# Performance work log

Hardware: AMD Instinct MI355X
Metric: run time of the kernel (lower is better)

## Reference

```python
import jax, jax.numpy as jnp
import numpy as np

N_NODES = 100000
N_EDGES = 6400000
PENALTY_N = 0.1  # init arg `n`


def setup_inputs() -> dict:
    key = jax.random.key(0)
    k1, k2, k3, k4, k5 = jax.random.split(key, 5)
    edge_index = jax.random.randint(k1, (2, N_EDGES), 0, N_NODES, dtype=jnp.int64 if jax.config.read('jax_enable_x64') else jnp.int32)
    edge_weight = jax.random.uniform(k2, (N_EDGES,), dtype=jnp.float32)
    nodes_yield_rate = jax.random.uniform(k3, (N_NODES,), dtype=jnp.float32)
    nodes_traffic = jax.random.uniform(k4, (N_NODES,), dtype=jnp.float32)
    nodes_cost = jax.random.uniform(k5, (N_NODES,), dtype=jnp.float32)
    return {
        'edge_index': edge_index,
        'edge_weight': edge_weight,
        'nodes_yield_rate': nodes_yield_rate,
        'nodes_traffic': nodes_traffic,
        'nodes_cost': nodes_cost,
    }


def reference(edge_index, edge_weight, nodes_yield_rate, nodes_traffic, nodes_cost):
    # Original loop reads src/dst traffic from the ORIGINAL tensor and accumulates
    # updates into a clone; both branches are equivalent to:
    #   src -= |diff| * n * w ; dst += |diff| * n * w
    # i.e. a pure per-edge scatter-add with no edge-order dependency.
    src = edge_index[0]
    dst = edge_index[1]
    diff = nodes_traffic[src] - nodes_traffic[dst]          # [E]
    transfer = jnp.abs(diff) * PENALTY_N * edge_weight      # [E]
    new_traffic = nodes_traffic.at[src].add(-transfer).at[dst].add(transfer)
    total_service_efficiency = jnp.sum(nodes_yield_rate * new_traffic - nodes_cost)
    return new_traffic, total_service_efficiency
```

## Files before the change

### kernel.cpp

```cpp
#include <hip/hip_runtime.h>

#define PENALTY_N 0.1f
#define CP 33344
#define HPAD 64
#define MAX_BPP 85
#define ABLK 1024

__global__ __launch_bounds__(ABLK, 4) void part_scatter_kernel(
    const int* __restrict__ src_idx,
    const int* __restrict__ dst_idx,
    const float* __restrict__ w,
    const float* __restrict__ traffic,
    float* __restrict__ scratch,
    float* __restrict__ out_scalar,
    int nE, int nN, int Bpp) {
    __shared__ float hist[CP + HPAD];

    const int p = blockIdx.x / Bpp;
    const int b = blockIdx.x % Bpp;
    const int lo = p * CP;
    const unsigned csz = (unsigned)min(CP, nN - lo);
    const int tid = threadIdx.x;

    if (blockIdx.x == 0 && tid == 0) *out_scalar = 0.0f;

    {
        float4* h4 = (float4*)hist;
        const int n4 = (CP + HPAD) / 4;
        for (int i = tid; i < n4; i += ABLK)
            h4[i] = make_float4(0.f, 0.f, 0.f, 0.f);
    }
    __syncthreads();

    const int nvec = nE >> 2;
    const int4* __restrict__ src4 = (const int4*)src_idx;
    const int4* __restrict__ dst4 = (const int4*)dst_idx;
    const float4* __restrict__ w4 = (const float4*)w;
    const int stride = Bpp * ABLK;

    for (int v = b * ABLK + tid; v < nvec; v += stride) {
        int4 s = src4[v];
        int4 d = dst4[v];
        float4 ww = w4[v];

        #pragma unroll
        for (int k = 0; k < 4; ++k) {
            int si = (&s.x)[k];
            int di = (&d.x)[k];
            unsigned so = (unsigned)(si - lo);
            unsigned doo = (unsigned)(di - lo);
            bool inS = so < csz;
            bool inD = doo < csz;
            if (inS || inD) {
                float t = fabsf(traffic[si] - traffic[di]) * (PENALTY_N * (&ww.x)[k]);
                unsigned iS = inS ? so : (unsigned)CP;
                unsigned iD = inD ? doo : (unsigned)CP;
                atomicAdd(&hist[iS], -t);
                atomicAdd(&hist[iD], t);
            }
        }
    }
    for (int e = (nvec << 2) + b * ABLK + tid; e < nE; e += stride) {
        int si = src_idx[e];
        int di = dst_idx[e];
        unsigned so = (unsigned)(si - lo);
        unsigned doo = (unsigned)(di - lo);
        bool inS = so < csz;
        bool inD = doo < csz;
        if (inS || inD) {
            float t = fabsf(traffic[si] - traffic[di]) * (PENALTY_N * w[e]);
            unsigned iS = inS ? so : (unsigned)CP;
            unsigned iD = inD ? doo : (unsigned)CP;
            atomicAdd(&hist[iS], -t);
            atomicAdd(&hist[iD], t);
        }
    }

    __syncthreads();
    float* dst = scratch + (size_t)blockIdx.x * CP;
    {
        const int n4 = (int)(csz >> 2);
        float4* d4 = (float4*)dst;
        const float4* h4 = (const float4*)hist;
        for (int i = tid; i < n4; i += ABLK) d4[i] = h4[i];
        for (int i = (n4 << 2) + tid; i < (int)csz; i += ABLK) dst[i] = hist[i];
    }
}

__global__ __launch_bounds__(256) void part_reduce_kernel(
    const float* __restrict__ scratch,
    const float* __restrict__ traffic,
    const float* __restrict__ yield_rate,
    const float* __restrict__ cost,
    float* __restrict__ out,
    int nN, int Bpp) {
    const int tid = blockIdx.x * blockDim.x + threadIdx.x;
    const int stride = gridDim.x * blockDim.x;

    float acc = 0.0f;
    for (int i = tid; i < nN; i += stride) {
        int p = i / CP;
        int off = i - p * CP;
        const float* base = scratch + (size_t)p * Bpp * CP + off;

        float s0 = traffic[i], s1 = 0.0f, s2 = 0.0f, s3 = 0.0f;
        int b = 0;
        for (; b + 8 <= Bpp; b += 8) {
            const float* q = base + (size_t)b * CP;
            float a0 = q[0 * (size_t)CP];
            float a1 = q[1 * (size_t)CP];
            float a2 = q[2 * (size_t)CP];
            float a3 = q[3 * (size_t)CP];
            float a4 = q[4 * (size_t)CP];
            float a5 = q[5 * (size_t)CP];
            float a6 = q[6 * (size_t)CP];
            float a7 = q[7 * (size_t)CP];
            s0 += a0 + a4;
            s1 += a1 + a5;
            s2 += a2 + a6;
            s3 += a3 + a7;
        }
        for (; b < Bpp; ++b) s0 += base[(size_t)b * CP];
        float s = (s0 + s1) + (s2 + s3);
        out[i] = s;
        acc = fmaf(yield_rate[i], s, acc) - cost[i];
    }

    #pragma unroll
    for (int off = 32; off > 0; off >>= 1) acc += __shfl_down(acc, off, 64);

    __shared__ float wsum[4];
    const int lane = threadIdx.x & 63;
    const int wid = threadIdx.x >> 6;
    if (lane == 0) wsum[wid] = acc;
    __syncthreads();
    if (threadIdx.x == 0)
        atomicAdd(&out[nN], wsum[0] + wsum[1] + wsum[2] + wsum[3]);
}

__global__ void init_out_kernel(const float* __restrict__ traffic,
                                float* __restrict__ out, int nN) {
    int i = blockIdx.x * blockDim.x + threadIdx.x;
    if (i < nN) out[i] = traffic[i];
    else if (i == nN) out[i] = 0.0f;
}

__global__ __launch_bounds__(256) void edge_scatter_kernel(
    const int* __restrict__ src_idx, const int* __restrict__ dst_idx,
    const float* __restrict__ w, const float* __restrict__ traffic,
    float* __restrict__ out, int nE) {
    const int tid = blockIdx.x * blockDim.x + threadIdx.x;
    const int stride = gridDim.x * blockDim.x;
    for (int e = tid; e < nE; e += stride) {
        int s = src_idx[e];
        int d = dst_idx[e];
        float t = fabsf(traffic[s] - traffic[d]) * (PENALTY_N * w[e]);
        atomicAdd(&out[s], -t);
        atomicAdd(&out[d], t);
    }
}

__global__ __launch_bounds__(256) void reduce_kernel(
    const float* __restrict__ new_traffic, const float* __restrict__ yield_rate,
    const float* __restrict__ cost, float* __restrict__ total, int nN) {
    const int tid = blockIdx.x * blockDim.x + threadIdx.x;
    const int stride = gridDim.x * blockDim.x;
    float acc = 0.0f;
    for (int i = tid; i < nN; i += stride)
        acc = fmaf(yield_rate[i], new_traffic[i], acc) - cost[i];
    #pragma unroll
    for (int off = 32; off > 0; off >>= 1) acc += __shfl_down(acc, off, 64);
    __shared__ float wsum[4];
    const int lane = threadIdx.x & 63;
    const int wid = threadIdx.x >> 6;
    if (lane == 0) wsum[wid] = acc;
    __syncthreads();
    if (threadIdx.x == 0)
        atomicAdd(total, wsum[0] + wsum[1] + wsum[2] + wsum[3]);
}

extern "C" void kernel_launch(void* const* d_in, const int* in_sizes, int n_in,
                              void* d_out, int out_size, void* d_ws, size_t ws_size,
                              hipStream_t stream) {
    const int* edge_index = (const int*)d_in[0];
    const float* edge_weight = (const float*)d_in[1];
    const float* nodes_yield = (const float*)d_in[2];
    const float* nodes_traffic = (const float*)d_in[3];
    const float* nodes_cost = (const float*)d_in[4];
    float* out = (float*)d_out;

    const int nE = in_sizes[1];
    const int nN = in_sizes[2];
    const int* src_idx = edge_index;
    const int* dst_idx = edge_index + nE;

    const int P = (nN + CP - 1) / CP;
    int Bpp = (int)(ws_size / ((size_t)P * CP * sizeof(float)));
    if (Bpp > MAX_BPP) Bpp = MAX_BPP;

    if (Bpp >= 4 && P <= 8) {
        float* scratch = (float*)d_ws;
        part_scatter_kernel<<<P * Bpp, ABLK, 0, stream>>>(
            src_idx, dst_idx, edge_weight, nodes_traffic,
            scratch, out + nN, nE, nN, Bpp);
        int rgrid = (nN + 255) / 256;
        part_reduce_kernel<<<rgrid, 256, 0, stream>>>(
            scratch, nodes_traffic, nodes_yield, nodes_cost, out, nN, Bpp);
    } else {
        int grid = (nN + 1 + 255) / 256;
        init_out_kernel<<<grid, 256, 0, stream>>>(nodes_traffic, out, nN);
        edge_scatter_kernel<<<2048, 256, 0, stream>>>(src_idx, dst_idx,
                                                      edge_weight, nodes_traffic,
                                                      out, nE);
        reduce_kernel<<<256, 256, 0, stream>>>(out, nodes_yield, nodes_cost,
                                               out + nN, nN);
    }
}
```

Baseline: 227.4 us.

## Precompute per-edge transfer once in fp16 before partitioned scatter

Adds a kernel that computes each edge's transfer value once and stores it as half precision in workspace. The partitioned histogram scatter then reads this compact value instead of re-gathering node traffic and weights in every partition pass. This removes redundant gathers and weight reads across partitions, but adds an extra launch and buffer traffic, and fp16 storage reduces accuracy of transfers. It also lowers the maximum blocks per partition and drops the padding slot.

```diff
diff --git a/kernel.cpp b/kernel.cpp
--- a/kernel.cpp
+++ b/kernel.cpp
@@ -1,20 +1,62 @@
 #include <hip/hip_runtime.h>
+#include <hip/hip_fp16.h>
 
 #define PENALTY_N 0.1f
 #define CP 33344
-#define HPAD 64
-#define MAX_BPP 85
+#define MAX_BPP 80
 #define ABLK 1024
 
-__global__ __launch_bounds__(ABLK, 4) void part_scatter_kernel(
+__global__ __launch_bounds__(256, 8) void compute_t_kernel(
     const int* __restrict__ src_idx,
     const int* __restrict__ dst_idx,
     const float* __restrict__ w,
     const float* __restrict__ traffic,
+    __half* __restrict__ tbuf,
+    float* __restrict__ out_scalar,
+    int nE) {
+    const int tid = blockIdx.x * blockDim.x + threadIdx.x;
+    const int stride = gridDim.x * blockDim.x;
+    if (blockIdx.x == 0 && threadIdx.x == 0) *out_scalar = 0.0f;
+
+    const int nvec = nE >> 2;
+    const int4* __restrict__ s4p = (const int4*)src_idx;
+    const int4* __restrict__ d4p = (const int4*)dst_idx;
+    const float4* __restrict__ w4p = (const float4*)w;
+    uint2* __restrict__ t2p = (uint2*)tbuf;
+
+    for (int v = tid; v < nvec; v += stride) {
+        int4 s = s4p[v];
+        int4 d = d4p[v];
+        float4 ww = w4p[v];
+        float a0 = traffic[s.x], a1 = traffic[s.y];
+        float a2 = traffic[s.z], a3 = traffic[s.w];
+        float b0 = traffic[d.x], b1 = traffic[d.y];
+        float b2 = traffic[d.z], b3 = traffic[d.w];
+        float t0 = fabsf(a0 - b0) * (PENALTY_N * ww.x);
+        float t1 = fabsf(a1 - b1) * (PENALTY_N * ww.y);
+        float t2 = fabsf(a2 - b2) * (PENALTY_N * ww.z);
+        float t3 = fabsf(a3 - b3) * (PENALTY_N * ww.w);
+        __half2 h01 = __floats2half2_rn(t0, t1);
+        __half2 h23 = __floats2half2_rn(t2, t3);
+        uint2 pk;
+        pk.x = *(unsigned*)&h01;
+        pk.y = *(unsigned*)&h23;
+        t2p[v] = pk;
+    }
+    for (int e = (nvec << 2) + tid; e < nE; e += stride) {
+        float t = fabsf(traffic[src_idx[e]] - traffic[dst_idx[e]]) *
+                  (PENALTY_N * w[e]);
+        tbuf[e] = __float2half_rn(t);
+    }
+}
+
+__global__ __launch_bounds__(ABLK, 4) void part_scatter_kernel(
+    const int* __restrict__ src_idx,
+    const int* __restrict__ dst_idx,
+    const __half* __restrict__ tbuf,
     float* __restrict__ scratch,
-    float* __restrict__ out_scalar,
     int nE, int nN, int Bpp) {
-    __shared__ float hist[CP + HPAD];
+    __shared__ float hist[CP];
 
     const int p = blockIdx.x / Bpp;
     const int b = blockIdx.x % Bpp;
@@ -22,58 +64,43 @@
     const unsigned csz = (unsigned)min(CP, nN - lo);
     const int tid = threadIdx.x;
 
-    if (blockIdx.x == 0 && tid == 0) *out_scalar = 0.0f;
-
     {
         float4* h4 = (float4*)hist;
-        const int n4 = (CP + HPAD) / 4;
-        for (int i = tid; i < n4; i += ABLK)
+        for (int i = tid; i < CP / 4; i += ABLK)
             h4[i] = make_float4(0.f, 0.f, 0.f, 0.f);
     }
     __syncthreads();
 
     const int nvec = nE >> 2;
-    const int4* __restrict__ src4 = (const int4*)src_idx;
-    const int4* __restrict__ dst4 = (const int4*)dst_idx;
-    const float4* __restrict__ w4 = (const float4*)w;
+    const int4* __restrict__ s4p = (const int4*)src_idx;
+    const int4* __restrict__ d4p = (const int4*)dst_idx;
+    const uint2* __restrict__ t2p = (const uint2*)tbuf;
     const int stride = Bpp * ABLK;
 
     for (int v = b * ABLK + tid; v < nvec; v += stride) {
-        int4 s = src4[v];
-        int4 d = dst4[v];
-        float4 ww = w4[v];
-
-        #pragma unroll
-        for (int k = 0; k < 4; ++k) {
-            int si = (&s.x)[k];
-            int di = (&d.x)[k];
-            unsigned so = (unsigned)(si - lo);
-            unsigned doo = (unsigned)(di - lo);
-            bool inS = so < csz;
-            bool inD = doo < csz;
-            if (inS || inD) {
-                float t = fabsf(traffic[si] - traffic[di]) * (PENALTY_N * (&ww.x)[k]);
-                unsigned iS = inS ? so : (unsigned)CP;
-                unsigned iD = inD ? doo : (unsigned)CP;
-                atomicAdd(&hist[iS], -t);
-                atomicAdd(&hist[iD], t);
-            }
-        }
+        int4 s = s4p[v];
+        int4 d = d4p[v];
+        uint2 pk = t2p[v];
+        __half2 h01 = *(__half2*)&pk.x;
+        __half2 h23 = *(__half2*)&pk.y;
+        float t0 = __low2float(h01), t1 = __high2float(h01);
+        float t2 = __low2float(h23), t3 = __high2float(h23);
+
+        unsigned u;
+        u = (unsigned)(s.x - lo); if (u < csz) atomicAdd(&hist[u], -t0);
+        u = (unsigned)(d.x - lo); if (u < csz) atomicAdd(&hist[u],  t0);
+        u = (unsigned)(s.y - lo); if (u < csz) atomicAdd(&hist[u], -t1);
+        u = (unsigned)(d.y - lo); if (u < csz) atomicAdd(&hist[u],  t1);
+        u = (unsigned)(s.z - lo); if (u < csz) atomicAdd(&hist[u], -t2);
+        u = (unsigned)(d.z - lo); if (u < csz) atomicAdd(&hist[u],  t2);
+        u = (unsigned)(s.w - lo); if (u < csz) atomicAdd(&hist[u], -t3);
+        u = (unsigned)(d.w - lo); if (u < csz) atomicAdd(&hist[u],  t3);
     }
     for (int e = (nvec << 2) + b * ABLK + tid; e < nE; e += stride) {
-        int si = src_idx[e];
-        int di = dst_idx[e];
-        unsigned so = (unsigned)(si - lo);
-        unsigned doo = (unsigned)(di - lo);
-        bool inS = so < csz;
-        bool inD = doo < csz;
-        if (inS || inD) {
-            float t = fabsf(traffic[si] - traffic[di]) * (PENALTY_N * w[e]);
-            unsigned iS = inS ? so : (unsigned)CP;
-            unsigned iD = inD ? doo : (unsigned)CP;
-            atomicAdd(&hist[iS], -t);
-            atomicAdd(&hist[iD], t);
-        }
+        float t = __half2float(tbuf[e]);
+        unsigned u;
+        u = (unsigned)(src_idx[e] - lo); if (u < csz) atomicAdd(&hist[u], -t);
+        u = (unsigned)(dst_idx[e] - lo); if (u < csz) atomicAdd(&hist[u],  t);
     }
 
     __syncthreads();
@@ -195,14 +222,21 @@
     const int* dst_idx = edge_index + nE;
 
     const int P = (nN + CP - 1) / CP;
-    int Bpp = (int)(ws_size / ((size_t)P * CP * sizeof(float)));
+
+    size_t tbytes = (((size_t)nE * sizeof(__half)) + 255) & ~(size_t)255;
+    size_t rem = (ws_size > tbytes) ? (ws_size - tbytes) : 0;
+    int Bpp = (int)(rem / ((size_t)P * CP * sizeof(float)));
     if (Bpp > MAX_BPP) Bpp = MAX_BPP;
 
-    if (Bpp >= 4 && P <= 8) {
-        float* scratch = (float*)d_ws;
+    if (Bpp >= 16 && P <= 8) {
+        __half* tbuf = (__half*)d_ws;
+        float* scratch = (float*)((char*)d_ws + tbytes);
+
+        compute_t_kernel<<<2048, 256, 0, stream>>>(
+            src_idx, dst_idx, edge_weight, nodes_traffic,
+            tbuf, out + nN, nE);
         part_scatter_kernel<<<P * Bpp, ABLK, 0, stream>>>(
-            src_idx, dst_idx, edge_weight, nodes_traffic,
-            scratch, out + nN, nE, nN, Bpp);
+            src_idx, dst_idx, tbuf, scratch, nE, nN, Bpp);
         int rgrid = (nN + 255) / 256;
         part_reduce_kernel<<<rgrid, 256, 0, stream>>>(
             scratch, nodes_traffic, nodes_yield, nodes_cost, out, nN, Bpp);
```

Result: slower. 235.5 us (+3.6%).

## Bin edge updates into fp16-packed partition buckets before shared-memory scatter

Applied to the files above, without the earlier changes.

Replaces the multi-pass partitioned scatter, where every partition block re-read all edges and traffic gathers, with a single pass that computes each edge's transfer once. That pass writes packed (local index, fp16 value) records into per-partition global buckets via block-local staging and atomic cursors. A second kernel streams each bucket into shared-memory histograms. This aims to cut redundant edge reads and gathers, at the cost of extra bucket write/read traffic, fp16 rounding of transfer values, and silent drops if a bucket overflows its capacity.

```diff
diff --git a/kernel.cpp b/kernel.cpp
--- a/kernel.cpp
+++ b/kernel.cpp
@@ -1,80 +1,155 @@
 #include <hip/hip_runtime.h>
+#include <hip/hip_fp16.h>
 
 #define PENALTY_N 0.1f
-#define CP 33344
-#define HPAD 64
-#define MAX_BPP 85
-#define ABLK 1024
-
-__global__ __launch_bounds__(ABLK, 4) void part_scatter_kernel(
+#define NPART 4
+#define CP 25024
+#define CBLK 256
+#define NW 4
+#define FL 512
+#define SBLK 1024
+#define MAX_BPP 64
+
+__global__ void init_kernel(unsigned* __restrict__ cursors,
+                            float* __restrict__ out_scalar) {
+    if (threadIdx.x < NPART) cursors[threadIdx.x] = 0u;
+    if (threadIdx.x == NPART) *out_scalar = 0.0f;
+}
+
+__global__ __launch_bounds__(CBLK, 4) void compute_bucket_kernel(
     const int* __restrict__ src_idx,
     const int* __restrict__ dst_idx,
     const float* __restrict__ w,
     const float* __restrict__ traffic,
+    unsigned* __restrict__ gbuckets,
+    unsigned* __restrict__ cursors,
+    int nE, unsigned bcap) {
+    __shared__ unsigned sbuf[NPART][NW][FL];
+    __shared__ unsigned scnt[NW][NPART];
+    __shared__ unsigned sbase[NPART];
+
+    const int tid = threadIdx.x;
+    const int wid = tid >> 6;
+    const int ngroups = (nE + 3) >> 2;
+    const int gstep = gridDim.x * CBLK;
+
+    const int4* __restrict__ s4p = (const int4*)src_idx;
+    const int4* __restrict__ d4p = (const int4*)dst_idx;
+    const float4* __restrict__ w4p = (const float4*)w;
+
+    for (int base = blockIdx.x * CBLK; base < ngroups; base += gstep) {
+        __syncthreads();
+        if (tid < NW * NPART) ((unsigned*)scnt)[tid] = 0u;
+        __syncthreads();
+
+        const int v = base + tid;
+        if (v < ngroups) {
+            const int e0 = v << 2;
+            int4 s, d;
+            float4 ww;
+            if (e0 + 3 < nE) {
+                s = s4p[v];
+                d = d4p[v];
+                ww = w4p[v];
+            } else {
+                int sa[4], da[4];
+                float wa[4];
+                for (int k = 0; k < 4; ++k) {
+                    int e = e0 + k;
+                    sa[k] = (e < nE) ? src_idx[e] : 0;
+                    da[k] = (e < nE) ? dst_idx[e] : 0;
+                    wa[k] = (e < nE) ? w[e] : 0.0f;
+                }
+                s = make_int4(sa[0], sa[1], sa[2], sa[3]);
+                d = make_int4(da[0], da[1], da[2], da[3]);
+                ww = make_float4(wa[0], wa[1], wa[2], wa[3]);
+            }
+            float a0 = traffic[s.x], a1 = traffic[s.y];
+            float a2 = traffic[s.z], a3 = traffic[s.w];
+            float b0 = traffic[d.x], b1 = traffic[d.y];
+            float b2 = traffic[d.z], b3 = traffic[d.w];
+            float t0 = fabsf(a0 - b0) * (PENALTY_N * ww.x);
+            float t1 = fabsf(a1 - b1) * (PENALTY_N * ww.y);
+            float t2 = fabsf(a2 - b2) * (PENALTY_N * ww.z);
+            float t3 = fabsf(a3 - b3) * (PENALTY_N * ww.w);
+
+#define STAGE(GI, VAL)                                                        \
+            {                                                                 \
+                unsigned gb_ = (unsigned)(GI) / (unsigned)CP;                 \
+                unsigned lc_ = (unsigned)(GI) - gb_ * (unsigned)CP;           \
+                unsigned hb_ =                                                \
+                    (unsigned)__half_as_ushort(__float2half_rn(VAL));         \
+                unsigned pos_ = atomicAdd(&scnt[wid][gb_], 1u);               \
+                sbuf[gb_][wid][pos_] = lc_ | (hb_ << 16);                     \
+            }
+            STAGE(s.x, -t0) STAGE(d.x, t0)
+            if (e0 + 1 < nE) { STAGE(s.y, -t1) STAGE(d.y, t1) }
+            if (e0 + 2 < nE) { STAGE(s.z, -t2) STAGE(d.z, t2) }
+            if (e0 + 3 < nE) { STAGE(s.w, -t3) STAGE(d.w, t3) }
+#undef STAGE
+        }
+        __syncthreads();
+        if (tid < NPART) {
+            unsigned tot = scnt[0][tid] + scnt[1][tid] +
+                           scnt[2][tid] + scnt[3][tid];
+            sbase[tid] = atomicAdd(&cursors[tid], tot);
+        }
+        __syncthreads();
+        for (int k = 0; k < NPART; ++k) {
+            unsigned off = 0;
+            unsigned* gk = gbuckets + (size_t)k * bcap;
+            for (int wv = 0; wv < NW; ++wv) {
+                unsigned c = scnt[wv][k];
+                unsigned gb = sbase[k] + off;
+                for (unsigned i = tid; i < c; i += CBLK) {
+                    unsigned gi = gb + i;
+                    if (gi < bcap) gk[gi] = sbuf[k][wv][i];
+                }
+                off += c;
+            }
+        }
+    }
+}
+
+__global__ __launch_bounds__(SBLK, 4) void bucket_scatter_kernel(
+    const unsigned* __restrict__ gbuckets,
+    const unsigned* __restrict__ cursors,
     float* __restrict__ scratch,
-    float* __restrict__ out_scalar,
-    int nE, int nN, int Bpp) {
-    __shared__ float hist[CP + HPAD];
+    int nN, int Bpp, unsigned bcap) {
+    __shared__ float hist[CP];
 
     const int p = blockIdx.x / Bpp;
-    const int b = blockIdx.x % Bpp;
-    const int lo = p * CP;
-    const unsigned csz = (unsigned)min(CP, nN - lo);
+    const int slice = blockIdx.x % Bpp;
     const int tid = threadIdx.x;
-
-    if (blockIdx.x == 0 && tid == 0) *out_scalar = 0.0f;
+    const unsigned total = min(cursors[p], bcap);
+    const unsigned csz = (unsigned)min(CP, nN - p * CP);
 
     {
         float4* h4 = (float4*)hist;
-        const int n4 = (CP + HPAD) / 4;
-        for (int i = tid; i < n4; i += ABLK)
+        for (int i = tid; i < CP / 4; i += SBLK)
             h4[i] = make_float4(0.f, 0.f, 0.f, 0.f);
     }
     __syncthreads();
 
-    const int nvec = nE >> 2;
-    const int4* __restrict__ src4 = (const int4*)src_idx;
-    const int4* __restrict__ dst4 = (const int4*)dst_idx;
-    const float4* __restrict__ w4 = (const float4*)w;
-    const int stride = Bpp * ABLK;
-
-    for (int v = b * ABLK + tid; v < nvec; v += stride) {
-        int4 s = src4[v];
-        int4 d = dst4[v];
-        float4 ww = w4[v];
-
-        #pragma unroll
-        for (int k = 0; k < 4; ++k) {
-            int si = (&s.x)[k];
-            int di = (&d.x)[k];
-            unsigned so = (unsigned)(si - lo);
-            unsigned doo = (unsigned)(di - lo);
-            bool inS = so < csz;
-            bool inD = doo < csz;
-            if (inS || inD) {
-                float t = fabsf(traffic[si] - traffic[di]) * (PENALTY_N * (&ww.x)[k]);
-                unsigned iS = inS ? so : (unsigned)CP;
-                unsigned iD = inD ? doo : (unsigned)CP;
-                atomicAdd(&hist[iS], -t);
-                atomicAdd(&hist[iD], t);
-            }
-        }
-    }
-    for (int e = (nvec << 2) + b * ABLK + tid; e < nE; e += stride) {
-        int si = src_idx[e];
-        int di = dst_idx[e];
-        unsigned so = (unsigned)(si - lo);
-        unsigned doo = (unsigned)(di - lo);
-        bool inS = so < csz;
-        bool inD = doo < csz;
-        if (inS || inD) {
-            float t = fabsf(traffic[si] - traffic[di]) * (PENALTY_N * w[e]);
-            unsigned iS = inS ? so : (unsigned)CP;
-            unsigned iD = inD ? doo : (unsigned)CP;
-            atomicAdd(&hist[iS], -t);
-            atomicAdd(&hist[iD], t);
-        }
-    }
+    const unsigned* __restrict__ bp = gbuckets + (size_t)p * bcap;
+    const uint4* __restrict__ b4 = (const uint4*)bp;
+    const unsigned nv4 = total >> 2;
+    const unsigned stride = (unsigned)(Bpp * SBLK);
+
+#define PROC(R)                                                               \
+    atomicAdd(&hist[(R) & 0xFFFFu],                                           \
+              __half2float(__ushort_as_half((unsigned short)((R) >> 16))));
+
+    for (unsigned i = (unsigned)(slice * SBLK + tid); i < nv4; i += stride) {
+        uint4 q = b4[i];
+        PROC(q.x) PROC(q.y) PROC(q.z) PROC(q.w)
+    }
+    for (unsigned e = (nv4 << 2) + (unsigned)(slice * SBLK + tid); e < total;
+         e += stride) {
+        unsigned r = bp[e];
+        PROC(r)
+    }
+#undef PROC
 
     __syncthreads();
     float* dst = scratch + (size_t)blockIdx.x * CP;
@@ -82,8 +157,8 @@
         const int n4 = (int)(csz >> 2);
         float4* d4 = (float4*)dst;
         const float4* h4 = (const float4*)hist;
-        for (int i = tid; i < n4; i += ABLK) d4[i] = h4[i];
-        for (int i = (n4 << 2) + tid; i < (int)csz; i += ABLK) dst[i] = hist[i];
+        for (int i = tid; i < n4; i += SBLK) d4[i] = h4[i];
+        for (int i = (n4 << 2) + tid; i < (int)csz; i += SBLK) dst[i] = hist[i];
     }
 }
 
@@ -194,17 +269,29 @@
     const int* src_idx = edge_index;
     const int* dst_idx = edge_index + nE;
 
-    const int P = (nN + CP - 1) / CP;
-    int Bpp = (int)(ws_size / ((size_t)P * CP * sizeof(float)));
+    size_t bcap = ((size_t)nE * 2u) / NPART;
+    bcap += bcap / 10;
+    bcap = (bcap + 1023) & ~(size_t)1023;
+    size_t bucket_bytes = bcap * sizeof(unsigned) * NPART;
+
+    size_t rem = (ws_size > bucket_bytes + 256)
+                     ? (ws_size - bucket_bytes - 256) : 0;
+    int Bpp = (int)(rem / ((size_t)NPART * CP * sizeof(float)));
     if (Bpp > MAX_BPP) Bpp = MAX_BPP;
 
-    if (Bpp >= 4 && P <= 8) {
-        float* scratch = (float*)d_ws;
-        part_scatter_kernel<<<P * Bpp, ABLK, 0, stream>>>(
+    if (Bpp >= 16 && nN <= NPART * CP && bcap < 0x7FFFFFFFu) {
+        unsigned* gbuckets = (unsigned*)d_ws;
+        float* scratch = (float*)((char*)d_ws + bucket_bytes);
+        unsigned* cursors = (unsigned*)((char*)d_ws + bucket_bytes +
+                                        (size_t)NPART * Bpp * CP * sizeof(float));
+
+        init_kernel<<<1, 64, 0, stream>>>(cursors, out + nN);
+        compute_bucket_kernel<<<2048, CBLK, 0, stream>>>(
             src_idx, dst_idx, edge_weight, nodes_traffic,
-            scratch, out + nN, nE, nN, Bpp);
-        int rgrid = (nN + 255) / 256;
-        part_reduce_kernel<<<rgrid, 256, 0, stream>>>(
+            gbuckets, cursors, nE, (unsigned)bcap);
+        bucket_scatter_kernel<<<NPART * Bpp, SBLK, 0, stream>>>(
+            gbuckets, cursors, scratch, nN, Bpp, (unsigned)bcap);
+        part_reduce_kernel<<<(nN + 255) / 256, 256, 0, stream>>>(
             scratch, nodes_traffic, nodes_yield, nodes_cost, out, nN, Bpp);
     } else {
         int grid = (nN + 1 + 255) / 256;
```

Measured after the change: 263.1 us. 1.16x slower.
